# Kernel tuning notes

Measured on AMD Instinct MI355X. Metric: run time of the kernel, lower is better.

The kernel has to match this reference:

```python
import jax, jax.numpy as jnp
import numpy as np

EPS = 0.01  # Normalizer eps
N_NODES = 100000
N_EDGES = 1600000


def gcn_conv(x, edge_index, W, b, n_nodes):
    """PyG-style GCNConv: x @ W, symmetric-normalized aggregation with self-loops, + bias."""
    src = jnp.concatenate([edge_index[0], jnp.arange(n_nodes)])  # [E+N]
    dst = jnp.concatenate([edge_index[1], jnp.arange(n_nodes)])  # [E+N]
    h = x @ W  # [N, out]
    ones = jnp.ones_like(dst, dtype=h.dtype)
    deg = jax.ops.segment_sum(ones, dst, num_segments=n_nodes)  # [N]
    dinv = jnp.where(deg > 0, jax.lax.rsqrt(deg), 0.0)
    norm = dinv[src] * dinv[dst]  # [E+N]
    msgs = h[src] * norm[:, None]  # [E+N, out]  (largest intermediate)
    out = jax.ops.segment_sum(msgs, dst, num_segments=n_nodes)  # [N, out]
    return out + b


def setup_inputs() -> dict:
    key = jax.random.key(0)
    k = jax.random.split(key, 6)
    x = jax.random.normal(k[0], (N_NODES, 16), dtype=jnp.float32)
    edge_index = jax.random.randint(k[1], (2, N_EDGES), 0, N_NODES)
    W1 = jax.random.normal(k[2], (16, 64), dtype=jnp.float32) * 0.25
    b1 = jax.random.normal(k[3], (64,), dtype=jnp.float32) * 0.1
    W3 = jax.random.normal(k[4], (64, 32), dtype=jnp.float32) * 0.125
    b3 = jax.random.normal(k[5], (32,), dtype=jnp.float32) * 0.1
    return {"x": x, "edge_index": edge_index, "W1": W1, "b1": b1, "W3": W3, "b3": b3}


def reference(x, edge_index, W1, b1, W3, b3):
    n = x.shape[0]
    h = jax.nn.relu(gcn_conv(x, edge_index, W1, b1, n))
    h = jax.nn.relu(gcn_conv(h, edge_index, W3, b3, n))
    # Normalizer: sequential Welford observe over all nodes then normalize with
    # FINAL stats == population mean / clamped population variance.
    mean = h.mean(axis=0)  # [32]
    var = jnp.maximum(((h - mean) ** 2).mean(axis=0), EPS)  # [32]
    return (h - mean) * jax.lax.rsqrt(var)
```

## Files before the change

kernel.cpp:

```cpp
#include <hip/hip_runtime.h>
#include <hip/hip_fp16.h>

#define EPS 0.01f
#define SCAN_BS 512
#define NCHUNKS 256
#define BUCKET_SHIFT 9
#define BUCKET_SZ (1 << BUCKET_SHIFT)
#define STAGE_CAP 16384


__global__ __launch_bounds__(SCAN_BS) void k_scan_block(const int* __restrict__ in,
                                                        int* __restrict__ out,
                                                        int* __restrict__ bsum, int n) {
    __shared__ int sd[SCAN_BS];
    int t = threadIdx.x;
    int gid = blockIdx.x * SCAN_BS + t;
    int v = (gid < n) ? in[gid] : 0;
    sd[t] = v;
    __syncthreads();
    for (int off = 1; off < SCAN_BS; off <<= 1) {
        int x = (t >= off) ? sd[t - off] : 0;
        __syncthreads();
        sd[t] += x;
        __syncthreads();
    }
    if (gid < n) out[gid] = sd[t] - v;
    if (t == SCAN_BS - 1) bsum[blockIdx.x] = sd[t];
}

__global__ __launch_bounds__(SCAN_BS) void k_scan_tops(int* __restrict__ bsum, int nb) {
    __shared__ int sd[SCAN_BS];
    int t = threadIdx.x;
    int v = (t < nb) ? bsum[t] : 0;
    sd[t] = v;
    __syncthreads();
    for (int off = 1; off < SCAN_BS; off <<= 1) {
        int x = (t >= off) ? sd[t - off] : 0;
        __syncthreads();
        sd[t] += x;
        __syncthreads();
    }
    if (t < nb) bsum[t] = sd[t] - v;
}

__global__ __launch_bounds__(SCAN_BS) void k_scan_add(int* __restrict__ out,
                                                      const int* __restrict__ bsum, int n) {
    int gid = blockIdx.x * SCAN_BS + threadIdx.x;
    if (gid < n) out[gid] += bsum[blockIdx.x];
}


__global__ __launch_bounds__(256) void kA_bucket_hist(const int* __restrict__ dst,
                                                      int* __restrict__ bh, int e,
                                                      int nbuck, int ce) {
    extern __shared__ int hist[];
    int b = blockIdx.x, t = threadIdx.x;
    for (int i = t; i < nbuck; i += 256) hist[i] = 0;
    __syncthreads();
    int lo = b * ce, hi = min(lo + ce, e);
    for (int i = lo + t; i < hi; i += 256) atomicAdd(&hist[dst[i] >> BUCKET_SHIFT], 1);
    __syncthreads();
    for (int i = t; i < nbuck; i += 256) bh[i * NCHUNKS + b] = hist[i];
}

__global__ __launch_bounds__(256) void kC_bucket_scatter(const int* __restrict__ src,
                                                         const int* __restrict__ dst,
                                                         const int* __restrict__ bhs,
                                                         unsigned int* __restrict__ eb, int e,
                                                         int nbuck, int ce) {
    extern __shared__ int cur[];
    int b = blockIdx.x, t = threadIdx.x;
    for (int i = t; i < nbuck; i += 256) cur[i] = bhs[i * NCHUNKS + b];
    __syncthreads();
    int lo = b * ce, hi = min(lo + ce, e);
    for (int i = lo + t; i < hi; i += 256) {
        int s = src[i], d = dst[i];
        int pos = atomicAdd(&cur[d >> BUCKET_SHIFT], 1);
        eb[pos] = ((unsigned int)(d & (BUCKET_SZ - 1)) << 23) | (unsigned int)s;
    }
}

__global__ __launch_bounds__(256) void kDeg_fill_prescale(const unsigned int* __restrict__ eb,
                                                          const int* __restrict__ bhs,
                                                          const float* __restrict__ x,
                                                          int* __restrict__ degi,
                                                          float* __restrict__ dinv,
                                                          int* __restrict__ rowstart,
                                                          int* __restrict__ csr_src,
                                                          __half* __restrict__ xs,
                                                          float* __restrict__ partial,
                                                          int n, int nbuck, int e) {
    __shared__ unsigned int ebs[STAGE_CAP];
    __shared__ int hist[BUCKET_SZ];
    __shared__ int ps[256];
    __shared__ float dv[BUCKET_SZ];
    int k = blockIdx.x, t = threadIdx.x;
    if (k == 0 && t < 64) partial[t] = 0.f;
    for (int i = t; i < BUCKET_SZ; i += 256) hist[i] = 0;
    __syncthreads();
    int lo = bhs[k * NCHUNKS];
    int hi = (k + 1 < nbuck) ? bhs[(k + 1) * NCHUNKS] : e;
    int cnt = hi - lo;
    bool fits = (cnt <= STAGE_CAP);
    for (int i = t; i < cnt; i += 256) {
        unsigned int p = eb[lo + i];
        if (fits) ebs[i] = p;
        atomicAdd(&hist[p >> 23], 1);
    }
    __syncthreads();
    int a0 = hist[2 * t], a1 = hist[2 * t + 1];
    ps[t] = a0 + a1;
    __syncthreads();
    for (int off = 1; off < 256; off <<= 1) {
        int v = (t >= off) ? ps[t - off] : 0;
        __syncthreads();
        ps[t] += v;
        __syncthreads();
    }
    int excl = ps[t] - (a0 + a1);
    int node0 = k << BUCKET_SHIFT;
    int rs0 = lo + excl, rs1 = lo + excl + a0;
    {
        int nd0 = node0 + 2 * t, nd1 = nd0 + 1;
        float d0 = rsqrtf((float)a0 + 1.0f);
        float d1 = rsqrtf((float)a1 + 1.0f);
        dv[2 * t] = d0;
        dv[2 * t + 1] = d1;
        if (nd0 < n) {
            degi[nd0] = a0;
            dinv[nd0] = d0;
            rowstart[nd0] = rs0;
        }
        if (nd1 < n) {
            degi[nd1] = a1;
            dinv[nd1] = d1;
            rowstart[nd1] = rs1;
        }
    }
    __syncthreads();
    hist[2 * t] = rs0;
    hist[2 * t + 1] = rs1;
    {
        const float2* xf2 = (const float2*)x;
        __half2* xs2 = (__half2*)xs;
        for (int i = t; i < BUCKET_SZ * 8; i += 256) {
            int rl = i >> 3;
            int node = node0 + rl;
            if (node < n) {
                float2 vv = xf2[(size_t)node * 8 + (i & 7)];
                float d = dv[rl];
                xs2[(size_t)node * 8 + (i & 7)] = __floats2half2_rn(vv.x * d, vv.y * d);
            }
        }
    }
    __syncthreads();
    for (int i = t; i < cnt; i += 256) {
        unsigned int p = fits ? ebs[i] : eb[lo + i];
        int dl = (int)(p >> 23);
        int s = (int)(p & 0x7fffffu);
        int pos = atomicAdd(&hist[dl], 1);
        csr_src[pos] = s;
    }
}


__global__ __launch_bounds__(256) void k_l1_fused(const int* __restrict__ rowstart,
                                                  const int* __restrict__ degi,
                                                  const int* __restrict__ csr_src,
                                                  const float* __restrict__ dinv,
                                                  const __half* __restrict__ xs,
                                                  const float* __restrict__ W1,
                                                  const float* __restrict__ b1,
                                                  const float* __restrict__ W3,
                                                  __half* __restrict__ h2s, int n) {
    __shared__ float w1[16 * 64];
    __shared__ float w3[64 * 32];
    __shared__ float bs[64];
    __shared__ __align__(16) float a[16 * 16];
    __shared__ float z[16 * 64];
    int t = threadIdx.x;
    for (int i = t; i < 16 * 64; i += 256) w1[i] = W1[i];
    for (int i = t; i < 64 * 32; i += 256) w3[i] = W3[i];
    if (t < 64) bs[t] = b1[t];

    int row0 = blockIdx.x * 16;
    int wv = t >> 6;
    int lane = t & 63;
    int c2 = lane & 7;
    int slot = lane >> 3;
    const __half2* xs2 = (const __half2*)xs;

    int nb = row0 + wv * 4;
    int node = nb;
    int rs_c = 0, dg_c = 0;
    if (node < n) { rs_c = rowstart[node]; dg_c = degi[node]; }
    for (int nid = 0; nid < 4; ++nid) {
        int node_nxt = nb + nid + 1;
        int rs_n = 0, dg_n = 0;
        if (nid < 3 && node_nxt < n) { rs_n = rowstart[node_nxt]; dg_n = degi[node_nxt]; }
        if (node < n) {
            float dn = dinv[node];
            float2 self = __half22float2(xs2[(size_t)node * 8 + c2]);
            const int* sp = csr_src + rs_c;
            int deg = dg_c;
            int L = (deg + 7) >> 3;
            int base = slot * L;
            int end = min(base + L, deg);
            float ax = 0.f, ay = 0.f, bx = 0.f, by = 0.f;
            int k = base;
            for (; k + 2 <= end; k += 2) {
                int s0 = sp[k], s1 = sp[k + 1];
                float2 v0 = __half22float2(xs2[(size_t)s0 * 8 + c2]);
                float2 v1 = __half22float2(xs2[(size_t)s1 * 8 + c2]);
                ax += v0.x; ay += v0.y;
                bx += v1.x; by += v1.y;
            }
            if (k < end) {
                int s0 = sp[k];
                float2 v0 = __half22float2(xs2[(size_t)s0 * 8 + c2]);
                ax += v0.x; ay += v0.y;
            }
            float sx = ax + bx, sy = ay + by;
            sx += __shfl_xor(sx, 8);  sy += __shfl_xor(sy, 8);
            sx += __shfl_xor(sx, 16); sy += __shfl_xor(sy, 16);
            sx += __shfl_xor(sx, 32); sy += __shfl_xor(sy, 32);
            if (slot == 0) {
                int r = wv * 4 + nid;
                ((float2*)(a + r * 16))[c2] = make_float2(dn * (sx + self.x), dn * (sy + self.y));
            }
        }
        node = node_nxt; rs_c = rs_n; dg_c = dg_n;
    }
    __syncthreads();

    for (int i = t; i < 1024; i += 256) {
        int r = i >> 6, c = i & 63;
        float acc = bs[c];
#pragma unroll
        for (int k = 0; k < 16; ++k) acc += a[r * 16 + k] * w1[k * 64 + c];
        z[i] = acc > 0.f ? acc : 0.f;
    }
    __syncthreads();
    for (int i = t; i < 512; i += 256) {
        int r = i >> 5, c = i & 31;
        float acc = 0.f;
#pragma unroll
        for (int k = 0; k < 64; ++k) acc += z[r * 64 + k] * w3[k * 32 + c];
        int row = row0 + r;
        if (row < n) h2s[(size_t)row * 32 + c] = __float2half(acc * dinv[row]);
    }
}


__global__ __launch_bounds__(256) void k_gather32_stats(const int* __restrict__ rowstart,
                                                        const int* __restrict__ degi,
                                                        const int* __restrict__ csr_src,
                                                        const float* __restrict__ dinv,
                                                        const __half* __restrict__ h2s,
                                                        const float* __restrict__ b3,
                                                        float* __restrict__ out,
                                                        float* __restrict__ partial, int n) {
    int t = threadIdx.x;
    int lane = t & 63;
    int c2 = lane & 15;
    int slot = lane >> 4;
    const __half2* h2 = (const __half2*)h2s;
    float2 bias = ((const float2*)b3)[c2];
    float s_x = 0.f, s_y = 0.f, q_x = 0.f, q_y = 0.f;

    int node = blockIdx.x * 32 + (t >> 6);
    int rs_c = 0, dg_c = 0;
    if (node < n) { rs_c = rowstart[node]; dg_c = degi[node]; }
    for (int it = 0; it < 8; ++it) {
        int node_nxt = node + 4;
        int rs_n = 0, dg_n = 0;
        if (it < 7 && node_nxt < n) { rs_n = rowstart[node_nxt]; dg_n = degi[node_nxt]; }
        if (node < n) {
            float dn = dinv[node];
            float2 self = __half22float2(h2[(size_t)node * 16 + c2]);
            const int* sp = csr_src + rs_c;
            int deg = dg_c;
            int L = (deg + 3) >> 2;
            int base = slot * L;
            int end = min(base + L, deg);
            float ax = 0.f, ay = 0.f, bx = 0.f, by = 0.f;
            float cx = 0.f, cy = 0.f, dx = 0.f, dy = 0.f;
            int k = base;
            for (; k + 4 <= end; k += 4) {
                int s0 = sp[k], s1 = sp[k + 1], s2 = sp[k + 2], s3 = sp[k + 3];
                float2 v0 = __half22float2(h2[(size_t)s0 * 16 + c2]);
                float2 v1 = __half22float2(h2[(size_t)s1 * 16 + c2]);
                float2 v2 = __half22float2(h2[(size_t)s2 * 16 + c2]);
                float2 v3 = __half22float2(h2[(size_t)s3 * 16 + c2]);
                ax += v0.x; ay += v0.y;
                bx += v1.x; by += v1.y;
                cx += v2.x; cy += v2.y;
                dx += v3.x; dy += v3.y;
            }
            for (; k < end; ++k) {
                int s0 = sp[k];
                float2 v0 = __half22float2(h2[(size_t)s0 * 16 + c2]);
                ax += v0.x; ay += v0.y;
            }
            float sx = (ax + bx) + (cx + dx);
            float sy = (ay + by) + (cy + dy);
            sx += __shfl_xor(sx, 16); sy += __shfl_xor(sy, 16);
            sx += __shfl_xor(sx, 32); sy += __shfl_xor(sy, 32);
            if (slot == 0) {
                float vx = dn * (sx + self.x) + bias.x;
                float vy = dn * (sy + self.y) + bias.y;
                vx = vx > 0.f ? vx : 0.f;
                vy = vy > 0.f ? vy : 0.f;
                ((float2*)(out + (size_t)node * 32))[c2] = make_float2(vx, vy);
                s_x += vx; s_y += vy;
                q_x += vx * vx; q_y += vy * vy;
            }
        }
        node = node_nxt; rs_c = rs_n; dg_c = dg_n;
    }
    __shared__ float ls[128], lq[128];
    int wv = t >> 6;
    if ((t & 63) < 16) {
        ls[wv * 32 + 2 * c2] = s_x;
        ls[wv * 32 + 2 * c2 + 1] = s_y;
        lq[wv * 32 + 2 * c2] = q_x;
        lq[wv * 32 + 2 * c2 + 1] = q_y;
    }
    __syncthreads();
    if (t < 32) {
        float a = 0.f, b = 0.f;
#pragma unroll
        for (int w = 0; w < 4; ++w) {
            a += ls[w * 32 + t];
            b += lq[w * 32 + t];
        }
        atomicAdd(&partial[t], a);
        atomicAdd(&partial[32 + t], b);
    }
}


__global__ void k_norm(float* __restrict__ h, const float* __restrict__ partial, int n) {
    __shared__ __align__(16) float mv[64];
    int t = threadIdx.x;
    if (t < 32) {
        float invn = 1.0f / (float)n;
        float mean = partial[t] * invn;
        float var = partial[32 + t] * invn - mean * mean;
        var = var > EPS ? var : EPS;
        mv[t] = mean;
        mv[32 + t] = rsqrtf(var);
    }
    __syncthreads();
    int idx = blockIdx.x * blockDim.x + threadIdx.x;
    if (idx < n * 8) {
        int c4 = idx & 7;
        float4 v = ((float4*)h)[idx];
        float4 m = ((const float4*)mv)[c4];
        float4 iv = ((const float4*)(mv + 32))[c4];
        v.x = (v.x - m.x) * iv.x;
        v.y = (v.y - m.y) * iv.y;
        v.z = (v.z - m.z) * iv.z;
        v.w = (v.w - m.w) * iv.w;
        ((float4*)h)[idx] = v;
    }
}

extern "C" void kernel_launch(void* const* d_in, const int* in_sizes, int n_in,
                              void* d_out, int out_size, void* d_ws, size_t ws_size,
                              hipStream_t stream) {
    const float* x  = (const float*)d_in[0];
    const int* ei   = (const int*)d_in[1];
    const float* W1 = (const float*)d_in[2];
    const float* b1 = (const float*)d_in[3];
    const float* W3 = (const float*)d_in[4];
    const float* b3 = (const float*)d_in[5];

    const int N = in_sizes[0] / 16;
    const int E = in_sizes[1] / 2;
    const int* src = ei;
    const int* dst = ei + E;

    const int NBUCK = (N + BUCKET_SZ - 1) >> BUCKET_SHIFT;
    const int CE = (E + NCHUNKS - 1) / NCHUNKS;
    const int BH_TOTAL = NBUCK * NCHUNKS;

    char* ws = (char*)d_ws;
    int*   degi     = (int*)ws;          ws += (size_t)N * 4;
    float* dinv     = (float*)ws;        ws += (size_t)N * 4;
    int*   rowstart = (int*)ws;          ws += (size_t)N * 4;
    int*   bsum2    = (int*)ws;          ws += (size_t)SCAN_BS * 4;
    int*   bh       = (int*)ws;          ws += (size_t)BH_TOTAL * 4;
    int*   bhs      = (int*)ws;          ws += (size_t)BH_TOTAL * 4;
    unsigned int* eb = (unsigned int*)ws; ws += (size_t)E * 4;
    int*   csr_src  = (int*)ws;          ws += (size_t)E * 4;
    __half* xs      = (__half*)ws;       ws += (size_t)N * 16 * 2;
    __half* h2s     = (__half*)ws;       ws += (size_t)N * 32 * 2;
    float* partial  = (float*)ws;        ws += 64 * 4;

    float* out = (float*)d_out;

    const int NB2 = (BH_TOTAL + SCAN_BS - 1) / SCAN_BS;

    kA_bucket_hist<<<NCHUNKS, 256, NBUCK * 4, stream>>>(dst, bh, E, NBUCK, CE);
    k_scan_block<<<NB2, SCAN_BS, 0, stream>>>(bh, bhs, bsum2, BH_TOTAL);
    k_scan_tops<<<1, SCAN_BS, 0, stream>>>(bsum2, NB2);
    k_scan_add<<<NB2, SCAN_BS, 0, stream>>>(bhs, bsum2, BH_TOTAL);
    kC_bucket_scatter<<<NCHUNKS, 256, NBUCK * 4, stream>>>(src, dst, bhs, eb, E, NBUCK, CE);

    kDeg_fill_prescale<<<NBUCK, 256, 0, stream>>>(eb, bhs, x, degi, dinv, rowstart,
                                                  csr_src, xs, partial, N, NBUCK, E);

    k_l1_fused<<<(N + 15) / 16, 256, 0, stream>>>(rowstart, degi, csr_src, dinv, xs,
                                                  W1, b1, W3, h2s, N);

    k_gather32_stats<<<(N + 31) / 32, 256, 0, stream>>>(rowstart, degi, csr_src, dinv, h2s,
                                                        b3, out, partial, N);

    k_norm<<<(N * 8 + 255) / 256, 256, 0, stream>>>(out, partial, N);
}
```

Before: 179.2 us.

## Halve dst-bucket size and vectorize edge loads in histogram/scatter kernels

Bucket size for the destination-bucketed CSR build is halved from 512 to 256 nodes, so the per-bucket fill kernel has one node per thread, uses a smaller LDS staging buffer, and launches twice as many blocks. The histogram and scatter kernels now read src/dst four at a time via int4 loads, with chunk sizes rounded to multiples of four for alignment. The aim is more parallelism and occupancy in the fill stage and fewer load instructions in the edge passes. In exchange there are more buckets, a larger bucket-histogram scan, and a higher chance that a bucket overflows the staging buffer and falls back to global reads.

Measured after the change: 167.6 us (median of 3 runs). 1.07x faster.

```diff
diff --git a/kernel.cpp b/kernel.cpp
--- a/kernel.cpp
+++ b/kernel.cpp
@@ -4,9 +4,9 @@
 #define EPS 0.01f
 #define SCAN_BS 512
 #define NCHUNKS 256
-#define BUCKET_SHIFT 9
+#define BUCKET_SHIFT 8
 #define BUCKET_SZ (1 << BUCKET_SHIFT)
-#define STAGE_CAP 16384
+#define STAGE_CAP 6144
 
 
 __global__ __launch_bounds__(SCAN_BS) void k_scan_block(const int* __restrict__ in,
@@ -58,7 +58,19 @@
     for (int i = t; i < nbuck; i += 256) hist[i] = 0;
     __syncthreads();
     int lo = b * ce, hi = min(lo + ce, e);
-    for (int i = lo + t; i < hi; i += 256) atomicAdd(&hist[dst[i] >> BUCKET_SHIFT], 1);
+    int len = hi - lo;
+    if (len > 0) {
+        int len4 = len & ~3;
+        for (int i = t * 4; i < len4; i += 1024) {
+            int4 d4 = *(const int4*)(dst + lo + i);
+            atomicAdd(&hist[d4.x >> BUCKET_SHIFT], 1);
+            atomicAdd(&hist[d4.y >> BUCKET_SHIFT], 1);
+            atomicAdd(&hist[d4.z >> BUCKET_SHIFT], 1);
+            atomicAdd(&hist[d4.w >> BUCKET_SHIFT], 1);
+        }
+        for (int i = len4 + t; i < len; i += 256)
+            atomicAdd(&hist[dst[lo + i] >> BUCKET_SHIFT], 1);
+    }
     __syncthreads();
     for (int i = t; i < nbuck; i += 256) bh[i * NCHUNKS + b] = hist[i];
 }
@@ -73,10 +85,26 @@
     for (int i = t; i < nbuck; i += 256) cur[i] = bhs[i * NCHUNKS + b];
     __syncthreads();
     int lo = b * ce, hi = min(lo + ce, e);
-    for (int i = lo + t; i < hi; i += 256) {
-        int s = src[i], d = dst[i];
-        int pos = atomicAdd(&cur[d >> BUCKET_SHIFT], 1);
-        eb[pos] = ((unsigned int)(d & (BUCKET_SZ - 1)) << 23) | (unsigned int)s;
+    int len = hi - lo;
+    if (len > 0) {
+        int len4 = len & ~3;
+        for (int i = t * 4; i < len4; i += 1024) {
+            int4 s4 = *(const int4*)(src + lo + i);
+            int4 d4 = *(const int4*)(dst + lo + i);
+            int p0 = atomicAdd(&cur[d4.x >> BUCKET_SHIFT], 1);
+            eb[p0] = ((unsigned int)(d4.x & (BUCKET_SZ - 1)) << 23) | (unsigned int)s4.x;
+            int p1 = atomicAdd(&cur[d4.y >> BUCKET_SHIFT], 1);
+            eb[p1] = ((unsigned int)(d4.y & (BUCKET_SZ - 1)) << 23) | (unsigned int)s4.y;
+            int p2 = atomicAdd(&cur[d4.z >> BUCKET_SHIFT], 1);
+            eb[p2] = ((unsigned int)(d4.z & (BUCKET_SZ - 1)) << 23) | (unsigned int)s4.z;
+            int p3 = atomicAdd(&cur[d4.w >> BUCKET_SHIFT], 1);
+            eb[p3] = ((unsigned int)(d4.w & (BUCKET_SZ - 1)) << 23) | (unsigned int)s4.w;
+        }
+        for (int i = len4 + t; i < len; i += 256) {
+            int s = src[lo + i], d = dst[lo + i];
+            int pos = atomicAdd(&cur[d >> BUCKET_SHIFT], 1);
+            eb[pos] = ((unsigned int)(d & (BUCKET_SZ - 1)) << 23) | (unsigned int)s;
+        }
     }
 }
 
@@ -92,11 +120,11 @@
                                                           int n, int nbuck, int e) {
     __shared__ unsigned int ebs[STAGE_CAP];
     __shared__ int hist[BUCKET_SZ];
-    __shared__ int ps[256];
+    __shared__ int ps[BUCKET_SZ];
     __shared__ float dv[BUCKET_SZ];
     int k = blockIdx.x, t = threadIdx.x;
     if (k == 0 && t < 64) partial[t] = 0.f;
-    for (int i = t; i < BUCKET_SZ; i += 256) hist[i] = 0;
+    hist[t] = 0;
     __syncthreads();
     int lo = bhs[k * NCHUNKS];
     int hi = (k + 1 < nbuck) ? bhs[(k + 1) * NCHUNKS] : e;
@@ -108,8 +136,8 @@
         atomicAdd(&hist[p >> 23], 1);
     }
     __syncthreads();
-    int a0 = hist[2 * t], a1 = hist[2 * t + 1];
-    ps[t] = a0 + a1;
+    int a0 = hist[t];
+    ps[t] = a0;
     __syncthreads();
     for (int off = 1; off < 256; off <<= 1) {
         int v = (t >= off) ? ps[t - off] : 0;
@@ -117,29 +145,21 @@
         ps[t] += v;
         __syncthreads();
     }
-    int excl = ps[t] - (a0 + a1);
+    int excl = ps[t] - a0;
     int node0 = k << BUCKET_SHIFT;
-    int rs0 = lo + excl, rs1 = lo + excl + a0;
+    int rs0 = lo + excl;
+    float d0 = rsqrtf((float)a0 + 1.0f);
+    dv[t] = d0;
     {
-        int nd0 = node0 + 2 * t, nd1 = nd0 + 1;
-        float d0 = rsqrtf((float)a0 + 1.0f);
-        float d1 = rsqrtf((float)a1 + 1.0f);
-        dv[2 * t] = d0;
-        dv[2 * t + 1] = d1;
-        if (nd0 < n) {
-            degi[nd0] = a0;
-            dinv[nd0] = d0;
-            rowstart[nd0] = rs0;
-        }
-        if (nd1 < n) {
-            degi[nd1] = a1;
-            dinv[nd1] = d1;
-            rowstart[nd1] = rs1;
-        }
-    }
-    __syncthreads();
-    hist[2 * t] = rs0;
-    hist[2 * t + 1] = rs1;
+        int nd = node0 + t;
+        if (nd < n) {
+            degi[nd] = a0;
+            dinv[nd] = d0;
+            rowstart[nd] = rs0;
+        }
+    }
+    __syncthreads();
+    hist[t] = rs0;
     {
         const float2* xf2 = (const float2*)x;
         __half2* xs2 = (__half2*)xs;
@@ -382,7 +402,8 @@
     const int* dst = ei + E;
 
     const int NBUCK = (N + BUCKET_SZ - 1) >> BUCKET_SHIFT;
-    const int CE = (E + NCHUNKS - 1) / NCHUNKS;
+    int CE = (E + NCHUNKS - 1) / NCHUNKS;
+    CE = (CE + 3) & ~3;
     const int BH_TOTAL = NBUCK * NCHUNKS;
 
     char* ws = (char*)d_ws;
```
